# Optimization experiments

Hardware: AMD Instinct MI355X
Metric: run time of the kernel (lower is better)

Reference implementation:

```python
import jax, jax.numpy as jnp
import numpy as np

B, N, E, H = 1, 4096, 256, 4
D = E // H  # 64


def setup_inputs() -> dict:
    key = jax.random.key(0)
    ks = jax.random.split(key, 16)
    s = lambda fan_in: 1.0 / np.sqrt(fan_in)
    inp = {
        "x": jax.random.normal(ks[0], (B, N, E), dtype=jnp.float32),
        "encoding": jax.random.normal(ks[1], (2, 1, 1, N, D), dtype=jnp.float32),
        # Wqkv: Linear(E, 3E)
        "Wqkv_w": jax.random.uniform(ks[2], (3 * E, E), jnp.float32, -s(E), s(E)),
        "Wqkv_b": jax.random.uniform(ks[3], (3 * E,), jnp.float32, -s(E), s(E)),
        # out_proj: Linear(E, E)
        "out_w": jax.random.uniform(ks[4], (E, E), jnp.float32, -s(E), s(E)),
        "out_b": jax.random.uniform(ks[5], (E,), jnp.float32, -s(E), s(E)),
        # ffn[0]: Linear(2E, 2E)
        "ffn1_w": jax.random.uniform(ks[6], (2 * E, 2 * E), jnp.float32, -s(2 * E), s(2 * E)),
        "ffn1_b": jax.random.uniform(ks[7], (2 * E,), jnp.float32, -s(2 * E), s(2 * E)),
        # ffn[1]: LayerNorm(2E)
        "ln_g": jnp.ones((2 * E,), jnp.float32),
        "ln_b": jnp.zeros((2 * E,), jnp.float32),
        # ffn[3]: Linear(2E, E)
        "ffn2_w": jax.random.uniform(ks[8], (E, 2 * E), jnp.float32, -s(2 * E), s(2 * E)),
        "ffn2_b": jax.random.uniform(ks[9], (E,), jnp.float32, -s(2 * E), s(2 * E)),
    }
    return inp


def _rotate_half(t):
    # t: (B, H, N, D) -> pairwise rotate along last dim
    t2 = t.reshape(B, H, -1, D // 2, 2)
    t2 = jnp.stack((-t2[..., 1], t2[..., 0]), axis=-1)
    return t2.reshape(B, H, -1, D)


def _layernorm(x, g, b, eps=1e-5):
    mu = jnp.mean(x, axis=-1, keepdims=True)
    var = jnp.mean(jnp.square(x - mu), axis=-1, keepdims=True)
    return (x - mu) * jax.lax.rsqrt(var + eps) * g + b


def reference(x, encoding, Wqkv_w, Wqkv_b, out_w, out_b,
              ffn1_w, ffn1_b, ln_g, ln_b, ffn2_w, ffn2_b):
    # fused QKV projection; last dim layout is (H, D, 3)
    qkv = x @ Wqkv_w.T + Wqkv_b                       # (B, N, 3E)
    qkv = qkv.reshape(B, N, H, D, 3).transpose(0, 2, 1, 3, 4)  # (B, H, N, D, 3)
    q, k, v = qkv[..., 0], qkv[..., 1], qkv[..., 2]
    # cached rotary embedding: t*cos + rotate_half(t)*sin
    q = q * encoding[0] + _rotate_half(q) * encoding[1]
    k = k * encoding[0] + _rotate_half(k) * encoding[1]
    # scaled dot-product attention (no mask)
    scores = jnp.einsum("bhqd,bhkd->bhqk", q, k) / np.sqrt(D).astype(np.float32)
    probs = jax.nn.softmax(scores, axis=-1)
    ctx = jnp.einsum("bhqk,bhkd->bhqd", probs, v)     # (B, H, N, D)
    ctx = ctx.transpose(0, 2, 1, 3).reshape(B, N, E)
    message = ctx @ out_w.T + out_b
    # concat-FFN with residual
    h = jnp.concatenate((x, message), axis=-1)        # (B, N, 2E)
    h = h @ ffn1_w.T + ffn1_b
    h = _layernorm(h, ln_g, ln_b)
    h = jax.nn.gelu(h, approximate=False)
    h = h @ ffn2_w.T + ffn2_b
    return x + h
```

## Files before the change

### kernel.cpp

```cpp
#include <hip/hip_runtime.h>
#include <math.h>

#define NTOK 4096
#define EMB  256
#define NH   4
#define HD   64

typedef unsigned short u16;
typedef __attribute__((ext_vector_type(8))) __bf16 bf16x8;
typedef __attribute__((ext_vector_type(4))) float f32x4;

__device__ __forceinline__ u16 f2bf(float f) {
    union { float f; unsigned u; } v; v.f = f;
    unsigned b = v.u;
    b += 0x7FFFu + ((b >> 16) & 1u);
    return (u16)(b >> 16);
}
__device__ __forceinline__ float bf2f(u16 u) {
    union { unsigned u; float f; } v; v.u = ((unsigned)u) << 16;
    return v.f;
}

__global__ __launch_bounds__(256) void prep(
    const float4* __restrict__ w0, const float4* __restrict__ w1,
    const float4* __restrict__ w2, const float4* __restrict__ w3,
    u16* __restrict__ wb,
    const float4* __restrict__ x4, u16* __restrict__ xb, u16* __restrict__ catb)
{
    const int bid = blockIdx.x;
    if (bid < 640) {
        const int f = bid * 256 + threadIdx.x;
        float4 v;
        if      (f <  49152) v = w0[f];
        else if (f <  65536) v = w1[f - 49152];
        else if (f < 131072) v = w2[f - 65536];
        else                 v = w3[f - 131072];
        uint2 o;
        o.x = (unsigned)f2bf(v.x) | ((unsigned)f2bf(v.y) << 16);
        o.y = (unsigned)f2bf(v.z) | ((unsigned)f2bf(v.w) << 16);
        *(uint2*)(wb + (size_t)f * 4) = o;
    } else {
        const int f = (bid - 640) * 256 + threadIdx.x;
        float4 v = x4[f];
        uint2 o;
        o.x = (unsigned)f2bf(v.x) | ((unsigned)f2bf(v.y) << 16);
        o.y = (unsigned)f2bf(v.z) | ((unsigned)f2bf(v.w) << 16);
        *(uint2*)(xb + (size_t)f * 4) = o;
        const int row = f >> 6, c = (f & 63) * 4;
        *(uint2*)(catb + (size_t)row * 512 + c) = o;
    }
}

__global__ __launch_bounds__(256) void gemm_bf16_abt(
    const u16* __restrict__ A,
    const u16* __restrict__ B,
    const float* __restrict__ bias,
    const float* __restrict__ resid, int ldr,
    float* __restrict__ Cf, u16* __restrict__ Cb, int ldc, int K)
{
    const int t = threadIdx.x, w = t >> 6, l = t & 63;
    const int lg = l >> 4, li = l & 15;
    const int row0 = blockIdx.y * 64 + w * 16;
    const int col0 = blockIdx.x * 64;

    f32x4 acc[4];
    #pragma unroll
    for (int nb = 0; nb < 4; ++nb) acc[nb] = (f32x4){0.f, 0.f, 0.f, 0.f};

    const u16* Ap = A + (size_t)(row0 + li) * K + lg * 8;
    const u16* Bp = B + (size_t)(col0 + li) * K + lg * 8;

    #pragma unroll 2
    for (int k0 = 0; k0 < K; k0 += 32) {
        bf16x8 a = *(const bf16x8*)(Ap + k0);
        #pragma unroll
        for (int nb = 0; nb < 4; ++nb) {
            bf16x8 b = *(const bf16x8*)(Bp + (size_t)nb * 16 * K + k0);
            acc[nb] = __builtin_amdgcn_mfma_f32_16x16x32_bf16(a, b, acc[nb], 0, 0, 0);
        }
    }

    #pragma unroll
    for (int nb = 0; nb < 4; ++nb) {
        const int col = col0 + nb * 16 + li;
        const float bs = bias[col];
        #pragma unroll
        for (int p = 0; p < 4; ++p) {
            const int row = row0 + lg * 4 + p;
            float v = acc[nb][p] + bs;
            if (resid) v += resid[(size_t)row * ldr + col];
            if (Cf) Cf[(size_t)row * ldc + col] = v;
            else    Cb[(size_t)row * ldc + col] = f2bf(v);
        }
    }
}

__global__ __launch_bounds__(256) void qkv_post(
    const u16* __restrict__ qkvb, const float* __restrict__ enc,
    unsigned* __restrict__ Qb, unsigned* __restrict__ Kb, u16* __restrict__ Vt)
{
    __shared__ u16 lds[64 * 66];
    const int bid = blockIdx.x;
    if (bid < 2048) {
        const int gid = bid * 256 + threadIdx.x;
        const int h   = gid >> 17;
        const int rem = gid & (NTOK * 32 - 1);
        const int n   = rem >> 5;
        const int p   = rem & 31;
        const int d0  = p * 2;

        const u16* base = qkvb + (size_t)n * 768 + h * 192 + d0 * 3;
        const float q0v = bf2f(base[0]), k0 = bf2f(base[1]);
        const float q1  = bf2f(base[3]), k1 = bf2f(base[4]);

        float2 c01 = *(const float2*)(enc + (size_t)n * 64 + d0);
        float2 s01 = *(const float2*)(enc + (size_t)NTOK * 64 + (size_t)n * 64 + d0);

        const float qo0 = (q0v * c01.x - q1 * s01.x) * 0.125f;
        const float qo1 = (q1 * c01.y + q0v * s01.y) * 0.125f;
        const float ko0 = k0 * c01.x - k1 * s01.x;
        const float ko1 = k1 * c01.y + k0 * s01.y;

        const size_t oidx = ((size_t)(h * NTOK + n) << 5) + p;
        Qb[oidx] = (unsigned)f2bf(qo0) | ((unsigned)f2bf(qo1) << 16);
        Kb[oidx] = (unsigned)f2bf(ko0) | ((unsigned)f2bf(ko1) << 16);
    } else {
        const int vb = bid - 2048;
        const int h  = vb >> 6;
        const int nt = vb & 63;
        const int t  = threadIdx.x;

        {
            const int nl = t & 63, dg = t >> 6;
            const u16* src = qkvb + (size_t)(nt * 64 + nl) * 768 + h * 192 + dg * 48 + 2;
            #pragma unroll
            for (int i = 0; i < 16; ++i)
                lds[(dg * 16 + i) * 66 + nl] = src[3 * i];
        }
        __syncthreads();
        {
            const int d = t >> 2, nc = t & 3;
            __align__(16) u16 us[16];
            #pragma unroll
            for (int i = 0; i < 16; ++i) us[i] = lds[d * 66 + nc * 16 + i];
            u16* dst = Vt + ((size_t)(h * 64 + d) << 12) + nt * 64 + nc * 16;
            *(uint4*)(dst)     = *(uint4*)(us);
            *(uint4*)(dst + 8) = *(uint4*)(us + 8);
        }
    }
}

__global__ __launch_bounds__(256, 4) void flash_attn_v4(
    const u16* __restrict__ Qb, const u16* __restrict__ Kb,
    const u16* __restrict__ Vt, u16* __restrict__ ctxb)
{
    __shared__ char  Plds[4 * 2048];
    __shared__ float Obuf[16 * 64];
    __shared__ float Mbuf[16], Lbuf[16];

    const int t  = threadIdx.x;
    const int wk = t >> 6;
    const int l  = t & 63;
    const int lg = l >> 4, li = l & 15;
    const int h  = blockIdx.y;
    const int q0 = blockIdx.x * 16;

    char* Pw = Plds + wk * 2048;

    bf16x8 QA[2];
    #pragma unroll
    for (int kh = 0; kh < 2; ++kh)
        QA[kh] = *(const bf16x8*)(Qb +
            ((size_t)(h * NTOK + q0 + li) << 6) + kh * 32 + lg * 8);

    f32x4 OA[4];
    float mrun[4], lrun[4];
    #pragma unroll
    for (int p = 0; p < 4; ++p) { mrun[p] = -1e30f; lrun[p] = 0.f; }
    #pragma unroll
    for (int db = 0; db < 4; ++db) OA[db] = (f32x4){0.f, 0.f, 0.f, 0.f};

    for (int it = 0; it < 16; ++it) {
        const int kt = (wk << 10) + (it << 6);

        bf16x8 KB[4][2], VB[4][2];
        #pragma unroll
        for (int kb = 0; kb < 4; ++kb)
            #pragma unroll
            for (int kh = 0; kh < 2; ++kh)
                KB[kb][kh] = *(const bf16x8*)(Kb +
                    ((size_t)(h * NTOK + kt + kb * 16 + li) << 6) + kh * 32 + lg * 8);
        #pragma unroll
        for (int db = 0; db < 4; ++db)
            #pragma unroll
            for (int kh = 0; kh < 2; ++kh)
                VB[db][kh] = *(const bf16x8*)(Vt +
                    ((size_t)(h * 64 + db * 16 + li) << 12) + kt + kh * 32 + lg * 8);

        f32x4 SA[4];
        #pragma unroll
        for (int kb = 0; kb < 4; ++kb) {
            f32x4 z = (f32x4){0.f, 0.f, 0.f, 0.f};
            z = __builtin_amdgcn_mfma_f32_16x16x32_bf16(QA[0], KB[kb][0], z, 0, 0, 0);
            SA[kb] = __builtin_amdgcn_mfma_f32_16x16x32_bf16(QA[1], KB[kb][1], z, 0, 0, 0);
        }

        #pragma unroll
        for (int p = 0; p < 4; ++p) {
            float mx = fmaxf(fmaxf(SA[0][p], SA[1][p]), fmaxf(SA[2][p], SA[3][p]));
            #pragma unroll
            for (int sh = 1; sh < 16; sh <<= 1)
                mx = fmaxf(mx, __shfl_xor(mx, sh));
            const float mo = mrun[p];
            const float mn = fmaxf(mo, mx);
            const float corr = __expf(mo - mn);
            mrun[p] = mn;
            float pv[4], ps = 0.f;
            #pragma unroll
            for (int kb = 0; kb < 4; ++kb) {
                pv[kb] = __expf(SA[kb][p] - mn);
                ps += pv[kb];
            }
            lrun[p] = lrun[p] * corr + ps;
            #pragma unroll
            for (int db = 0; db < 4; ++db) OA[db][p] *= corr;

            const int ql = lg * 4 + p;
            #pragma unroll
            for (int kb = 0; kb < 4; ++kb) {
                const int kl = kb * 16 + li;
                *(u16*)(Pw + ql * 128 + ((kl * 2) ^ ((ql & 7) << 4))) = f2bf(pv[kb]);
            }
        }

        #pragma unroll
        for (int kh = 0; kh < 2; ++kh) {
            const int ql = li;
            bf16x8 PA = *(const bf16x8*)(Pw + ql * 128 +
                            ((kh * 64 + lg * 16) ^ ((ql & 7) << 4)));
            #pragma unroll
            for (int db = 0; db < 4; ++db)
                OA[db] = __builtin_amdgcn_mfma_f32_16x16x32_bf16(
                    PA, VB[db][kh], OA[db], 0, 0, 0);
        }
    }

    #pragma unroll
    for (int p = 0; p < 4; ++p) {
        float ps = lrun[p];
        #pragma unroll
        for (int sh = 1; sh < 16; sh <<= 1) ps += __shfl_xor(ps, sh);
        lrun[p] = ps;
    }

    if (wk == 0) {
        #pragma unroll
        for (int p = 0; p < 4; ++p) {
            const int q = lg * 4 + p;
            #pragma unroll
            for (int db = 0; db < 4; ++db)
                Obuf[q * 64 + db * 16 + li] = OA[db][p];
            if (li == 0) { Mbuf[q] = mrun[p]; Lbuf[q] = lrun[p]; }
        }
    }
    #pragma unroll
    for (int wv = 1; wv < 4; ++wv) {
        __syncthreads();
        if (wk == wv) {
            #pragma unroll
            for (int p = 0; p < 4; ++p) {
                const int q = lg * 4 + p;
                const float Mo = Mbuf[q], Lo = Lbuf[q];
                const float mn = fmaxf(Mo, mrun[p]);
                const float a  = __expf(Mo - mn);
                const float b  = __expf(mrun[p] - mn);
                #pragma unroll
                for (int db = 0; db < 4; ++db) {
                    const int idx = q * 64 + db * 16 + li;
                    Obuf[idx] = Obuf[idx] * a + OA[db][p] * b;
                }
                if (li == 0) { Mbuf[q] = mn; Lbuf[q] = Lo * a + lrun[p] * b; }
            }
        }
    }
    __syncthreads();

    {
        const int q = t >> 4, dc = (t & 15) * 4;
        const float rl = 1.f / Lbuf[q];
        uint2 ov;
        ov.x = (unsigned)f2bf(Obuf[q * 64 + dc + 0] * rl) |
               ((unsigned)f2bf(Obuf[q * 64 + dc + 1] * rl) << 16);
        ov.y = (unsigned)f2bf(Obuf[q * 64 + dc + 2] * rl) |
               ((unsigned)f2bf(Obuf[q * 64 + dc + 3] * rl) << 16);
        *(uint2*)(ctxb + (size_t)(q0 + q) * EMB + h * 64 + dc) = ov;
    }
}

__global__ __launch_bounds__(256) void ln_gelu_v2(
    const u16* __restrict__ h1b, const float* __restrict__ g,
    const float* __restrict__ b, u16* __restrict__ h2b)
{
    const int wid = threadIdx.x >> 6, l = threadIdx.x & 63;
    const int row = blockIdx.x * 4 + wid;

    uint4 hv = *(const uint4*)(h1b + (size_t)row * 512 + l * 8);
    const unsigned* hw = (const unsigned*)&hv;
    float v[8];
    #pragma unroll
    for (int j = 0; j < 4; ++j) {
        v[2 * j]     = bf2f((u16)(hw[j] & 0xffff));
        v[2 * j + 1] = bf2f((u16)(hw[j] >> 16));
    }

    float s = 0.f;
    #pragma unroll
    for (int i = 0; i < 8; ++i) s += v[i];
    #pragma unroll
    for (int sh = 1; sh < 64; sh <<= 1) s += __shfl_xor(s, sh);
    const float mu = s * (1.f / 512.f);

    float d[8], vs = 0.f;
    #pragma unroll
    for (int i = 0; i < 8; ++i) { d[i] = v[i] - mu; vs += d[i] * d[i]; }
    #pragma unroll
    for (int sh = 1; sh < 64; sh <<= 1) vs += __shfl_xor(vs, sh);
    const float rstd = rsqrtf(vs * (1.f / 512.f) + 1e-5f);

    float4 g0 = *(const float4*)(g + l * 8);
    float4 g1 = *(const float4*)(g + l * 8 + 4);
    float4 b0 = *(const float4*)(b + l * 8);
    float4 b1 = *(const float4*)(b + l * 8 + 4);
    float gg[8] = {g0.x, g0.y, g0.z, g0.w, g1.x, g1.y, g1.z, g1.w};
    float bb[8] = {b0.x, b0.y, b0.z, b0.w, b1.x, b1.y, b1.z, b1.w};

    uint4 ov;
    unsigned* op = (unsigned*)&ov;
    #pragma unroll
    for (int j = 0; j < 4; ++j) {
        float y0 = d[2 * j] * rstd * gg[2 * j] + bb[2 * j];
        float y1 = d[2 * j + 1] * rstd * gg[2 * j + 1] + bb[2 * j + 1];
        float o0 = 0.5f * y0 * (1.f + erff(y0 * 0.70710678118654752f));
        float o1 = 0.5f * y1 * (1.f + erff(y1 * 0.70710678118654752f));
        op[j] = (unsigned)f2bf(o0) | ((unsigned)f2bf(o1) << 16);
    }
    *(uint4*)(h2b + (size_t)row * 512 + l * 8) = ov;
}

extern "C" void kernel_launch(void* const* d_in, const int* in_sizes, int n_in,
                              void* d_out, int out_size, void* d_ws, size_t ws_size,
                              hipStream_t stream)
{
    const float* x      = (const float*)d_in[0];
    const float* enc    = (const float*)d_in[1];
    const float* Wqkv_w = (const float*)d_in[2];
    const float* Wqkv_b = (const float*)d_in[3];
    const float* out_w  = (const float*)d_in[4];
    const float* out_b  = (const float*)d_in[5];
    const float* ffn1_w = (const float*)d_in[6];
    const float* ffn1_b = (const float*)d_in[7];
    const float* ln_g   = (const float*)d_in[8];
    const float* ln_b   = (const float*)d_in[9];
    const float* ffn2_w = (const float*)d_in[10];
    const float* ffn2_b = (const float*)d_in[11];
    float* out = (float*)d_out;
    float* ws  = (float*)d_ws;

    u16*   catb = (u16*)(ws);
    u16*   wb   = (u16*)(ws + 1048576);
    u16*   Qb   = (u16*)(ws + 1376256);
    u16*   Kb   = (u16*)(ws + 1900544);
    u16*   Vt   = (u16*)(ws + 2424832);
    u16*   ctxb = (u16*)(ws + 2949120);
    u16*   qkvb = (u16*)(ws + 3473408);
    u16*   h1b  = (u16*)(ws + 3473408);
    u16*   xb   = (u16*)(ws + 5570560);
    u16*   h2b  = (u16*)(ws + 5570560);

    u16* Wqkvb = wb;
    u16* outwb = wb + 196608;
    u16* ffn1b = wb + 262144;
    u16* ffn2b = wb + 524288;

    prep<<<1664, 256, 0, stream>>>((const float4*)Wqkv_w, (const float4*)out_w,
                                   (const float4*)ffn1_w, (const float4*)ffn2_w, wb,
                                   (const float4*)x, xb, catb);
    gemm_bf16_abt<<<dim3(12, 64), 256, 0, stream>>>(xb, Wqkvb, Wqkv_b,
                                                    nullptr, 0, nullptr, qkvb, 768, 256);
    qkv_post<<<2304, 256, 0, stream>>>(qkvb, enc, (unsigned*)Qb, (unsigned*)Kb, Vt);
    flash_attn_v4<<<dim3(256, NH), 256, 0, stream>>>(Qb, Kb, Vt, ctxb);
    gemm_bf16_abt<<<dim3(4, 64), 256, 0, stream>>>(ctxb, outwb, out_b,
                                                   nullptr, 0, nullptr, catb + 256, 512, 256);
    gemm_bf16_abt<<<dim3(8, 64), 256, 0, stream>>>(catb, ffn1b, ffn1_b,
                                                   nullptr, 0, nullptr, h1b, 512, 512);
    ln_gelu_v2<<<1024, 256, 0, stream>>>(h1b, ln_g, ln_b, h2b);
    gemm_bf16_abt<<<dim3(4, 64), 256, 0, stream>>>(h2b, ffn2b, ffn2_b,
                                                   x, 256, out, nullptr, 256, 512);
}
```

Measured before the change: 280.8 us.

## Double query tile per wave in attention and GEMM, add register prefetching

Flash attention now handles 32 query rows per block (two 16-row MFMA tiles per wave), so each K/V fragment loaded is reused twice, and it double-buffers the next K/V tile in registers. The GEMM likewise computes 128 rows per block with two A fragments per wave and register-prefetches the next K-slice. The output write is widened to 16-byte stores. This cuts global load traffic per FLOP and hides load latency, at the cost of more registers, lower occupancy (launch bounds 2 for attention), and half as many blocks.

New measurement: 229.2 us. 1.22x faster.

```diff
diff --git a/kernel.cpp b/kernel.cpp
--- a/kernel.cpp
+++ b/kernel.cpp
@@ -51,7 +51,7 @@
     }
 }
 
-__global__ __launch_bounds__(256) void gemm_bf16_abt(
+__global__ __launch_bounds__(256, 4) void gemm_bf16_v2(
     const u16* __restrict__ A,
     const u16* __restrict__ B,
     const float* __restrict__ bias,
@@ -60,39 +60,66 @@
 {
     const int t = threadIdx.x, w = t >> 6, l = t & 63;
     const int lg = l >> 4, li = l & 15;
-    const int row0 = blockIdx.y * 64 + w * 16;
+    const int row0 = blockIdx.y * 128 + w * 32;
     const int col0 = blockIdx.x * 64;
 
-    f32x4 acc[4];
-    #pragma unroll
-    for (int nb = 0; nb < 4; ++nb) acc[nb] = (f32x4){0.f, 0.f, 0.f, 0.f};
-
-    const u16* Ap = A + (size_t)(row0 + li) * K + lg * 8;
-    const u16* Bp = B + (size_t)(col0 + li) * K + lg * 8;
-
-    #pragma unroll 2
-    for (int k0 = 0; k0 < K; k0 += 32) {
-        bf16x8 a = *(const bf16x8*)(Ap + k0);
+    f32x4 acc[2][4];
+    #pragma unroll
+    for (int m = 0; m < 2; ++m)
+        #pragma unroll
+        for (int nb = 0; nb < 4; ++nb) acc[m][nb] = (f32x4){0.f, 0.f, 0.f, 0.f};
+
+    const u16* Ap0 = A + (size_t)(row0 + li) * K + lg * 8;
+    const u16* Ap1 = Ap0 + (size_t)16 * K;
+    const u16* Bp  = B + (size_t)(col0 + li) * K + lg * 8;
+
+    bf16x8 a0c = *(const bf16x8*)(Ap0);
+    bf16x8 a1c = *(const bf16x8*)(Ap1);
+    bf16x8 b0c = *(const bf16x8*)(Bp);
+    bf16x8 b1c = *(const bf16x8*)(Bp + (size_t)16 * K);
+    bf16x8 b2c = *(const bf16x8*)(Bp + (size_t)32 * K);
+    bf16x8 b3c = *(const bf16x8*)(Bp + (size_t)48 * K);
+    bf16x8 a0n, a1n, b0n, b1n, b2n, b3n;
+
+#define GSTEP(a0x,a1x,b0x,b1x,b2x,b3x, a0y,a1y,b0y,b1y,b2y,b3y, KC) do { \
+    const int kn_ = ((KC) + 32 < K) ? (KC) + 32 : (KC); \
+    a0y = *(const bf16x8*)(Ap0 + kn_); \
+    a1y = *(const bf16x8*)(Ap1 + kn_); \
+    b0y = *(const bf16x8*)(Bp + kn_); \
+    b1y = *(const bf16x8*)(Bp + (size_t)16 * K + kn_); \
+    b2y = *(const bf16x8*)(Bp + (size_t)32 * K + kn_); \
+    b3y = *(const bf16x8*)(Bp + (size_t)48 * K + kn_); \
+    acc[0][0] = __builtin_amdgcn_mfma_f32_16x16x32_bf16(a0x, b0x, acc[0][0], 0, 0, 0); \
+    acc[0][1] = __builtin_amdgcn_mfma_f32_16x16x32_bf16(a0x, b1x, acc[0][1], 0, 0, 0); \
+    acc[0][2] = __builtin_amdgcn_mfma_f32_16x16x32_bf16(a0x, b2x, acc[0][2], 0, 0, 0); \
+    acc[0][3] = __builtin_amdgcn_mfma_f32_16x16x32_bf16(a0x, b3x, acc[0][3], 0, 0, 0); \
+    acc[1][0] = __builtin_amdgcn_mfma_f32_16x16x32_bf16(a1x, b0x, acc[1][0], 0, 0, 0); \
+    acc[1][1] = __builtin_amdgcn_mfma_f32_16x16x32_bf16(a1x, b1x, acc[1][1], 0, 0, 0); \
+    acc[1][2] = __builtin_amdgcn_mfma_f32_16x16x32_bf16(a1x, b2x, acc[1][2], 0, 0, 0); \
+    acc[1][3] = __builtin_amdgcn_mfma_f32_16x16x32_bf16(a1x, b3x, acc[1][3], 0, 0, 0); \
+} while (0)
+
+    for (int k0 = 0; k0 < K; k0 += 64) {
+        GSTEP(a0c,a1c,b0c,b1c,b2c,b3c, a0n,a1n,b0n,b1n,b2n,b3n, k0);
+        GSTEP(a0n,a1n,b0n,b1n,b2n,b3n, a0c,a1c,b0c,b1c,b2c,b3c, k0 + 32);
+    }
+#undef GSTEP
+
+    #pragma unroll
+    for (int m = 0; m < 2; ++m)
         #pragma unroll
         for (int nb = 0; nb < 4; ++nb) {
-            bf16x8 b = *(const bf16x8*)(Bp + (size_t)nb * 16 * K + k0);
-            acc[nb] = __builtin_amdgcn_mfma_f32_16x16x32_bf16(a, b, acc[nb], 0, 0, 0);
+            const int col = col0 + nb * 16 + li;
+            const float bs = bias[col];
+            #pragma unroll
+            for (int p = 0; p < 4; ++p) {
+                const int row = row0 + m * 16 + lg * 4 + p;
+                float v = acc[m][nb][p] + bs;
+                if (resid) v += resid[(size_t)row * ldr + col];
+                if (Cf) Cf[(size_t)row * ldc + col] = v;
+                else    Cb[(size_t)row * ldc + col] = f2bf(v);
+            }
         }
-    }
-
-    #pragma unroll
-    for (int nb = 0; nb < 4; ++nb) {
-        const int col = col0 + nb * 16 + li;
-        const float bs = bias[col];
-        #pragma unroll
-        for (int p = 0; p < 4; ++p) {
-            const int row = row0 + lg * 4 + p;
-            float v = acc[nb][p] + bs;
-            if (resid) v += resid[(size_t)row * ldr + col];
-            if (Cf) Cf[(size_t)row * ldc + col] = v;
-            else    Cb[(size_t)row * ldc + col] = f2bf(v);
-        }
-    }
 }
 
 __global__ __launch_bounds__(256) void qkv_post(
@@ -150,150 +177,182 @@
     }
 }
 
-__global__ __launch_bounds__(256, 4) void flash_attn_v4(
+__global__ __launch_bounds__(256, 2) void flash_attn_v5(
     const u16* __restrict__ Qb, const u16* __restrict__ Kb,
     const u16* __restrict__ Vt, u16* __restrict__ ctxb)
 {
-    __shared__ char  Plds[4 * 2048];
-    __shared__ float Obuf[16 * 64];
-    __shared__ float Mbuf[16], Lbuf[16];
+    __shared__ char  Plds[4 * 4096];
+    __shared__ float Obuf[32 * 64];
+    __shared__ float Mbuf[32], Lbuf[32];
 
     const int t  = threadIdx.x;
     const int wk = t >> 6;
     const int l  = t & 63;
     const int lg = l >> 4, li = l & 15;
     const int h  = blockIdx.y;
-    const int q0 = blockIdx.x * 16;
-
-    char* Pw = Plds + wk * 2048;
-
-    bf16x8 QA[2];
-    #pragma unroll
-    for (int kh = 0; kh < 2; ++kh)
-        QA[kh] = *(const bf16x8*)(Qb +
-            ((size_t)(h * NTOK + q0 + li) << 6) + kh * 32 + lg * 8);
-
-    f32x4 OA[4];
-    float mrun[4], lrun[4];
-    #pragma unroll
-    for (int p = 0; p < 4; ++p) { mrun[p] = -1e30f; lrun[p] = 0.f; }
-    #pragma unroll
-    for (int db = 0; db < 4; ++db) OA[db] = (f32x4){0.f, 0.f, 0.f, 0.f};
-
-    for (int it = 0; it < 16; ++it) {
-        const int kt = (wk << 10) + (it << 6);
-
-        bf16x8 KB[4][2], VB[4][2];
+    const int q0 = blockIdx.x * 32;
+
+    char* Pw = Plds + wk * 4096;
+
+    bf16x8 QA[2][2];
+    #pragma unroll
+    for (int Mb = 0; Mb < 2; ++Mb)
+        #pragma unroll
+        for (int kh = 0; kh < 2; ++kh)
+            QA[Mb][kh] = *(const bf16x8*)(Qb +
+                ((size_t)(h * NTOK + q0 + Mb * 16 + li) << 6) + kh * 32 + lg * 8);
+
+    f32x4 OA[2][4];
+    float mrun[2][4], lrun[2][4];
+    #pragma unroll
+    for (int Mb = 0; Mb < 2; ++Mb) {
+        #pragma unroll
+        for (int p = 0; p < 4; ++p) { mrun[Mb][p] = -1e30f; lrun[Mb][p] = 0.f; }
+        #pragma unroll
+        for (int db = 0; db < 4; ++db) OA[Mb][db] = (f32x4){0.f, 0.f, 0.f, 0.f};
+    }
+
+    bf16x8 K0f[4][2], V0f[4][2], K1f[4][2], V1f[4][2];
+
+    {
+        const int kt0 = wk << 10;
         #pragma unroll
         for (int kb = 0; kb < 4; ++kb)
             #pragma unroll
-            for (int kh = 0; kh < 2; ++kh)
-                KB[kb][kh] = *(const bf16x8*)(Kb +
-                    ((size_t)(h * NTOK + kt + kb * 16 + li) << 6) + kh * 32 + lg * 8);
-        #pragma unroll
-        for (int db = 0; db < 4; ++db)
-            #pragma unroll
-            for (int kh = 0; kh < 2; ++kh)
-                VB[db][kh] = *(const bf16x8*)(Vt +
-                    ((size_t)(h * 64 + db * 16 + li) << 12) + kt + kh * 32 + lg * 8);
-
-        f32x4 SA[4];
-        #pragma unroll
-        for (int kb = 0; kb < 4; ++kb) {
-            f32x4 z = (f32x4){0.f, 0.f, 0.f, 0.f};
-            z = __builtin_amdgcn_mfma_f32_16x16x32_bf16(QA[0], KB[kb][0], z, 0, 0, 0);
-            SA[kb] = __builtin_amdgcn_mfma_f32_16x16x32_bf16(QA[1], KB[kb][1], z, 0, 0, 0);
+            for (int kh = 0; kh < 2; ++kh) {
+                K0f[kb][kh] = *(const bf16x8*)(Kb +
+                    ((size_t)(h * NTOK + kt0 + kb * 16 + li) << 6) + kh * 32 + lg * 8);
+                V0f[kb][kh] = *(const bf16x8*)(Vt +
+                    ((size_t)(h * 64 + kb * 16 + li) << 12) + kt0 + kh * 32 + lg * 8);
+            }
+    }
+
+#define FITER(KC, VC, KN, VN, IT) do { \
+    const int itn_ = ((IT) < 15) ? (IT) + 1 : (IT); \
+    const int ktn_ = (wk << 10) + (itn_ << 6); \
+    _Pragma("unroll") \
+    for (int kb = 0; kb < 4; ++kb) { \
+        _Pragma("unroll") \
+        for (int kh = 0; kh < 2; ++kh) { \
+            KN[kb][kh] = *(const bf16x8*)(Kb + \
+                ((size_t)(h * NTOK + ktn_ + kb * 16 + li) << 6) + kh * 32 + lg * 8); \
+            VN[kb][kh] = *(const bf16x8*)(Vt + \
+                ((size_t)(h * 64 + kb * 16 + li) << 12) + ktn_ + kh * 32 + lg * 8); \
+        } \
+    } \
+    f32x4 SA_[2][4]; \
+    _Pragma("unroll") \
+    for (int Mb = 0; Mb < 2; ++Mb) { \
+        _Pragma("unroll") \
+        for (int kb = 0; kb < 4; ++kb) { \
+            f32x4 z_ = (f32x4){0.f, 0.f, 0.f, 0.f}; \
+            z_ = __builtin_amdgcn_mfma_f32_16x16x32_bf16(QA[Mb][0], KC[kb][0], z_, 0, 0, 0); \
+            SA_[Mb][kb] = __builtin_amdgcn_mfma_f32_16x16x32_bf16(QA[Mb][1], KC[kb][1], z_, 0, 0, 0); \
+        } \
+    } \
+    _Pragma("unroll") \
+    for (int Mb = 0; Mb < 2; ++Mb) { \
+        _Pragma("unroll") \
+        for (int p = 0; p < 4; ++p) { \
+            float mx_ = fmaxf(fmaxf(SA_[Mb][0][p], SA_[Mb][1][p]), \
+                              fmaxf(SA_[Mb][2][p], SA_[Mb][3][p])); \
+            _Pragma("unroll") \
+            for (int sh = 1; sh < 16; sh <<= 1) mx_ = fmaxf(mx_, __shfl_xor(mx_, sh)); \
+            const float mo_ = mrun[Mb][p]; \
+            const float mn_ = fmaxf(mo_, mx_); \
+            const float corr_ = __expf(mo_ - mn_); \
+            mrun[Mb][p] = mn_; \
+            float pe0_ = __expf(SA_[Mb][0][p] - mn_); \
+            float pe1_ = __expf(SA_[Mb][1][p] - mn_); \
+            float pe2_ = __expf(SA_[Mb][2][p] - mn_); \
+            float pe3_ = __expf(SA_[Mb][3][p] - mn_); \
+            lrun[Mb][p] = lrun[Mb][p] * corr_ + (pe0_ + pe1_ + pe2_ + pe3_); \
+            _Pragma("unroll") \
+            for (int db = 0; db < 4; ++db) OA[Mb][db][p] *= corr_; \
+            const int ql_ = Mb * 16 + lg * 4 + p; \
+            *(u16*)(Pw + ql_ * 128 + (((0 * 16 + li) * 2) ^ ((ql_ & 7) << 4))) = f2bf(pe0_); \
+            *(u16*)(Pw + ql_ * 128 + (((1 * 16 + li) * 2) ^ ((ql_ & 7) << 4))) = f2bf(pe1_); \
+            *(u16*)(Pw + ql_ * 128 + (((2 * 16 + li) * 2) ^ ((ql_ & 7) << 4))) = f2bf(pe2_); \
+            *(u16*)(Pw + ql_ * 128 + (((3 * 16 + li) * 2) ^ ((ql_ & 7) << 4))) = f2bf(pe3_); \
+        } \
+    } \
+    _Pragma("unroll") \
+    for (int Mb = 0; Mb < 2; ++Mb) { \
+        _Pragma("unroll") \
+        for (int kh = 0; kh < 2; ++kh) { \
+            const int ql_ = Mb * 16 + li; \
+            bf16x8 PA_ = *(const bf16x8*)(Pw + ql_ * 128 + \
+                            ((kh * 64 + lg * 16) ^ ((ql_ & 7) << 4))); \
+            _Pragma("unroll") \
+            for (int db = 0; db < 4; ++db) \
+                OA[Mb][db] = __builtin_amdgcn_mfma_f32_16x16x32_bf16( \
+                    PA_, VC[db][kh], OA[Mb][db], 0, 0, 0); \
+        } \
+    } \
+} while (0)
+
+    for (int it = 0; it < 16; it += 2) {
+        FITER(K0f, V0f, K1f, V1f, it);
+        FITER(K1f, V1f, K0f, V0f, it + 1);
+    }
+#undef FITER
+
+    #pragma unroll
+    for (int Mb = 0; Mb < 2; ++Mb)
+        #pragma unroll
+        for (int p = 0; p < 4; ++p) {
+            float ps = lrun[Mb][p];
+            #pragma unroll
+            for (int sh = 1; sh < 16; sh <<= 1) ps += __shfl_xor(ps, sh);
+            lrun[Mb][p] = ps;
         }
 
-        #pragma unroll
-        for (int p = 0; p < 4; ++p) {
-            float mx = fmaxf(fmaxf(SA[0][p], SA[1][p]), fmaxf(SA[2][p], SA[3][p]));
-            #pragma unroll
-            for (int sh = 1; sh < 16; sh <<= 1)
-                mx = fmaxf(mx, __shfl_xor(mx, sh));
-            const float mo = mrun[p];
-            const float mn = fmaxf(mo, mx);
-            const float corr = __expf(mo - mn);
-            mrun[p] = mn;
-            float pv[4], ps = 0.f;
-            #pragma unroll
-            for (int kb = 0; kb < 4; ++kb) {
-                pv[kb] = __expf(SA[kb][p] - mn);
-                ps += pv[kb];
+    if (wk == 0) {
+        #pragma unroll
+        for (int Mb = 0; Mb < 2; ++Mb)
+            #pragma unroll
+            for (int p = 0; p < 4; ++p) {
+                const int q = Mb * 16 + lg * 4 + p;
+                #pragma unroll
+                for (int db = 0; db < 4; ++db)
+                    Obuf[q * 64 + db * 16 + li] = OA[Mb][db][p];
+                if (li == 0) { Mbuf[q] = mrun[Mb][p]; Lbuf[q] = lrun[Mb][p]; }
             }
-            lrun[p] = lrun[p] * corr + ps;
-            #pragma unroll
-            for (int db = 0; db < 4; ++db) OA[db][p] *= corr;
-
-            const int ql = lg * 4 + p;
-            #pragma unroll
-            for (int kb = 0; kb < 4; ++kb) {
-                const int kl = kb * 16 + li;
-                *(u16*)(Pw + ql * 128 + ((kl * 2) ^ ((ql & 7) << 4))) = f2bf(pv[kb]);
-            }
-        }
-
-        #pragma unroll
-        for (int kh = 0; kh < 2; ++kh) {
-            const int ql = li;
-            bf16x8 PA = *(const bf16x8*)(Pw + ql * 128 +
-                            ((kh * 64 + lg * 16) ^ ((ql & 7) << 4)));
-            #pragma unroll
-            for (int db = 0; db < 4; ++db)
-                OA[db] = __builtin_amdgcn_mfma_f32_16x16x32_bf16(
-                    PA, VB[db][kh], OA[db], 0, 0, 0);
-        }
-    }
-
-    #pragma unroll
-    for (int p = 0; p < 4; ++p) {
-        float ps = lrun[p];
-        #pragma unroll
-        for (int sh = 1; sh < 16; sh <<= 1) ps += __shfl_xor(ps, sh);
-        lrun[p] = ps;
-    }
-
-    if (wk == 0) {
-        #pragma unroll
-        for (int p = 0; p < 4; ++p) {
-            const int q = lg * 4 + p;
-            #pragma unroll
-            for (int db = 0; db < 4; ++db)
-                Obuf[q * 64 + db * 16 + li] = OA[db][p];
-            if (li == 0) { Mbuf[q] = mrun[p]; Lbuf[q] = lrun[p]; }
-        }
     }
     #pragma unroll
     for (int wv = 1; wv < 4; ++wv) {
         __syncthreads();
         if (wk == wv) {
             #pragma unroll
-            for (int p = 0; p < 4; ++p) {
-                const int q = lg * 4 + p;
-                const float Mo = Mbuf[q], Lo = Lbuf[q];
-                const float mn = fmaxf(Mo, mrun[p]);
-                const float a  = __expf(Mo - mn);
-                const float b  = __expf(mrun[p] - mn);
+            for (int Mb = 0; Mb < 2; ++Mb)
                 #pragma unroll
-                for (int db = 0; db < 4; ++db) {
-                    const int idx = q * 64 + db * 16 + li;
-                    Obuf[idx] = Obuf[idx] * a + OA[db][p] * b;
+                for (int p = 0; p < 4; ++p) {
+                    const int q = Mb * 16 + lg * 4 + p;
+                    const float Mo = Mbuf[q], Lo = Lbuf[q];
+                    const float mn = fmaxf(Mo, mrun[Mb][p]);
+                    const float a  = __expf(Mo - mn);
+                    const float b  = __expf(mrun[Mb][p] - mn);
+                    #pragma unroll
+                    for (int db = 0; db < 4; ++db) {
+                        const int idx = q * 64 + db * 16 + li;
+                        Obuf[idx] = Obuf[idx] * a + OA[Mb][db][p] * b;
+                    }
+                    if (li == 0) { Mbuf[q] = mn; Lbuf[q] = Lo * a + lrun[Mb][p] * b; }
                 }
-                if (li == 0) { Mbuf[q] = mn; Lbuf[q] = Lo * a + lrun[p] * b; }
-            }
         }
     }
     __syncthreads();
 
     {
-        const int q = t >> 4, dc = (t & 15) * 4;
+        const int q = t >> 3, dc = (t & 7) * 8;
         const float rl = 1.f / Lbuf[q];
-        uint2 ov;
-        ov.x = (unsigned)f2bf(Obuf[q * 64 + dc + 0] * rl) |
-               ((unsigned)f2bf(Obuf[q * 64 + dc + 1] * rl) << 16);
-        ov.y = (unsigned)f2bf(Obuf[q * 64 + dc + 2] * rl) |
-               ((unsigned)f2bf(Obuf[q * 64 + dc + 3] * rl) << 16);
-        *(uint2*)(ctxb + (size_t)(q0 + q) * EMB + h * 64 + dc) = ov;
+        uint4 ov;
+        unsigned* op = (unsigned*)&ov;
+        #pragma unroll
+        for (int i = 0; i < 8; i += 2)
+            op[i >> 1] = (unsigned)f2bf(Obuf[q * 64 + dc + i] * rl) |
+                         ((unsigned)f2bf(Obuf[q * 64 + dc + i + 1] * rl) << 16);
+        *(uint4*)(ctxb + (size_t)(q0 + q) * EMB + h * 64 + dc) = ov;
     }
 }
 
@@ -385,15 +444,15 @@
     prep<<<1664, 256, 0, stream>>>((const float4*)Wqkv_w, (const float4*)out_w,
                                    (const float4*)ffn1_w, (const float4*)ffn2_w, wb,
                                    (const float4*)x, xb, catb);
-    gemm_bf16_abt<<<dim3(12, 64), 256, 0, stream>>>(xb, Wqkvb, Wqkv_b,
-                                                    nullptr, 0, nullptr, qkvb, 768, 256);
+    gemm_bf16_v2<<<dim3(12, 32), 256, 0, stream>>>(xb, Wqkvb, Wqkv_b,
+                                                   nullptr, 0, nullptr, qkvb, 768, 256);
     qkv_post<<<2304, 256, 0, stream>>>(qkvb, enc, (unsigned*)Qb, (unsigned*)Kb, Vt);
-    flash_attn_v4<<<dim3(256, NH), 256, 0, stream>>>(Qb, Kb, Vt, ctxb);
-    gemm_bf16_abt<<<dim3(4, 64), 256, 0, stream>>>(ctxb, outwb, out_b,
-                                                   nullptr, 0, nullptr, catb + 256, 512, 256);
-    gemm_bf16_abt<<<dim3(8, 64), 256, 0, stream>>>(catb, ffn1b, ffn1_b,
-                                                   nullptr, 0, nullptr, h1b, 512, 512);
+    flash_attn_v5<<<dim3(128, NH), 256, 0, stream>>>(Qb, Kb, Vt, ctxb);
+    gemm_bf16_v2<<<dim3(4, 32), 256, 0, stream>>>(ctxb, outwb, out_b,
+                                                  nullptr, 0, nullptr, catb + 256, 512, 256);
+    gemm_bf16_v2<<<dim3(8, 32), 256, 0, stream>>>(catb, ffn1b, ffn1_b,
+                                                  nullptr, 0, nullptr, h1b, 512, 512);
     ln_gelu_v2<<<1024, 256, 0, stream>>>(h1b, ln_g, ln_b, h2b);
-    gemm_bf16_abt<<<dim3(4, 64), 256, 0, stream>>>(h2b, ffn2b, ffn2_b,
-                                                   x, 256, out, nullptr, 256, 512);
-}
+    gemm_bf16_v2<<<dim3(4, 32), 256, 0, stream>>>(h2b, ffn2b, ffn2_b,
+                                                  x, 256, out, nullptr, 256, 512);
+}
```

## Double-buffer GEMM operand loads and widen flash attention to 32 queries per block

Applied to the files above, without the earlier changes.

The GEMM loop now software-pipelines its global loads, fetching the next K-slice's A and B fragments into a second register set while MFMAs run on the current one. It also adds an occupancy hint to the launch bounds. The attention kernel goes to 512 threads covering 32 queries with 8 waves, so each K/V tile loaded by a key-split wave position serves two query groups across the block. V loads are moved after the QK^T MFMAs to shorten register live ranges. The costs are more registers for double buffering and twice the LDS per attention block, which may reduce occupancy.

Result: faster. 272.3 us (-3.0%).

```diff
diff --git a/kernel.cpp b/kernel.cpp
--- a/kernel.cpp
+++ b/kernel.cpp
@@ -51,7 +51,7 @@
     }
 }
 
-__global__ __launch_bounds__(256) void gemm_bf16_abt(
+__global__ __launch_bounds__(256, 4) void gemm_bf16_v3(
     const u16* __restrict__ A,
     const u16* __restrict__ B,
     const float* __restrict__ bias,
@@ -70,15 +70,31 @@
     const u16* Ap = A + (size_t)(row0 + li) * K + lg * 8;
     const u16* Bp = B + (size_t)(col0 + li) * K + lg * 8;
 
-    #pragma unroll 2
-    for (int k0 = 0; k0 < K; k0 += 32) {
-        bf16x8 a = *(const bf16x8*)(Ap + k0);
-        #pragma unroll
-        for (int nb = 0; nb < 4; ++nb) {
-            bf16x8 b = *(const bf16x8*)(Bp + (size_t)nb * 16 * K + k0);
-            acc[nb] = __builtin_amdgcn_mfma_f32_16x16x32_bf16(a, b, acc[nb], 0, 0, 0);
-        }
-    }
+    bf16x8 ac  = *(const bf16x8*)(Ap);
+    bf16x8 b0c = *(const bf16x8*)(Bp);
+    bf16x8 b1c = *(const bf16x8*)(Bp + (size_t)16 * K);
+    bf16x8 b2c = *(const bf16x8*)(Bp + (size_t)32 * K);
+    bf16x8 b3c = *(const bf16x8*)(Bp + (size_t)48 * K);
+    bf16x8 an, b0n, b1n, b2n, b3n;
+
+#define GSTEP(ax,b0x,b1x,b2x,b3x, ay,b0y,b1y,b2y,b3y, KC) do { \
+    const int kn_ = ((KC) + 32 < K) ? (KC) + 32 : (KC); \
+    ay  = *(const bf16x8*)(Ap + kn_); \
+    b0y = *(const bf16x8*)(Bp + kn_); \
+    b1y = *(const bf16x8*)(Bp + (size_t)16 * K + kn_); \
+    b2y = *(const bf16x8*)(Bp + (size_t)32 * K + kn_); \
+    b3y = *(const bf16x8*)(Bp + (size_t)48 * K + kn_); \
+    acc[0] = __builtin_amdgcn_mfma_f32_16x16x32_bf16(ax, b0x, acc[0], 0, 0, 0); \
+    acc[1] = __builtin_amdgcn_mfma_f32_16x16x32_bf16(ax, b1x, acc[1], 0, 0, 0); \
+    acc[2] = __builtin_amdgcn_mfma_f32_16x16x32_bf16(ax, b2x, acc[2], 0, 0, 0); \
+    acc[3] = __builtin_amdgcn_mfma_f32_16x16x32_bf16(ax, b3x, acc[3], 0, 0, 0); \
+} while (0)
+
+    for (int k0 = 0; k0 < K; k0 += 64) {
+        GSTEP(ac,b0c,b1c,b2c,b3c, an,b0n,b1n,b2n,b3n, k0);
+        GSTEP(an,b0n,b1n,b2n,b3n, ac,b0c,b1c,b2c,b3c, k0 + 32);
+    }
+#undef GSTEP
 
     #pragma unroll
     for (int nb = 0; nb < 4; ++nb) {
@@ -150,28 +166,29 @@
     }
 }
 
-__global__ __launch_bounds__(256, 4) void flash_attn_v4(
+__global__ __launch_bounds__(512, 4) void flash_attn_v6(
     const u16* __restrict__ Qb, const u16* __restrict__ Kb,
     const u16* __restrict__ Vt, u16* __restrict__ ctxb)
 {
-    __shared__ char  Plds[4 * 2048];
-    __shared__ float Obuf[16 * 64];
-    __shared__ float Mbuf[16], Lbuf[16];
+    __shared__ char  Plds[8 * 2048];
+    __shared__ float Obuf[32 * 64];
+    __shared__ float Mbuf[32], Lbuf[32];
 
     const int t  = threadIdx.x;
-    const int wk = t >> 6;
+    const int w  = t >> 6;
+    const int wq = w >> 2, wk = w & 3;
     const int l  = t & 63;
     const int lg = l >> 4, li = l & 15;
     const int h  = blockIdx.y;
-    const int q0 = blockIdx.x * 16;
-
-    char* Pw = Plds + wk * 2048;
+    const int q0 = blockIdx.x * 32;
+
+    char* Pw = Plds + w * 2048;
 
     bf16x8 QA[2];
     #pragma unroll
     for (int kh = 0; kh < 2; ++kh)
         QA[kh] = *(const bf16x8*)(Qb +
-            ((size_t)(h * NTOK + q0 + li) << 6) + kh * 32 + lg * 8);
+            ((size_t)(h * NTOK + q0 + wq * 16 + li) << 6) + kh * 32 + lg * 8);
 
     f32x4 OA[4];
     float mrun[4], lrun[4];
@@ -183,19 +200,13 @@
     for (int it = 0; it < 16; ++it) {
         const int kt = (wk << 10) + (it << 6);
 
-        bf16x8 KB[4][2], VB[4][2];
+        bf16x8 KB[4][2];
         #pragma unroll
         for (int kb = 0; kb < 4; ++kb)
             #pragma unroll
             for (int kh = 0; kh < 2; ++kh)
                 KB[kb][kh] = *(const bf16x8*)(Kb +
                     ((size_t)(h * NTOK + kt + kb * 16 + li) << 6) + kh * 32 + lg * 8);
-        #pragma unroll
-        for (int db = 0; db < 4; ++db)
-            #pragma unroll
-            for (int kh = 0; kh < 2; ++kh)
-                VB[db][kh] = *(const bf16x8*)(Vt +
-                    ((size_t)(h * 64 + db * 16 + li) << 12) + kt + kh * 32 + lg * 8);
 
         f32x4 SA[4];
         #pragma unroll
@@ -204,6 +215,14 @@
             z = __builtin_amdgcn_mfma_f32_16x16x32_bf16(QA[0], KB[kb][0], z, 0, 0, 0);
             SA[kb] = __builtin_amdgcn_mfma_f32_16x16x32_bf16(QA[1], KB[kb][1], z, 0, 0, 0);
         }
+
+        bf16x8 VB[4][2];
+        #pragma unroll
+        for (int db = 0; db < 4; ++db)
+            #pragma unroll
+            for (int kh = 0; kh < 2; ++kh)
+                VB[db][kh] = *(const bf16x8*)(Vt +
+                    ((size_t)(h * 64 + db * 16 + li) << 12) + kt + kh * 32 + lg * 8);
 
         #pragma unroll
         for (int p = 0; p < 4; ++p) {
@@ -256,7 +275,7 @@
     if (wk == 0) {
         #pragma unroll
         for (int p = 0; p < 4; ++p) {
-            const int q = lg * 4 + p;
+            const int q = wq * 16 + lg * 4 + p;
             #pragma unroll
             for (int db = 0; db < 4; ++db)
                 Obuf[q * 64 + db * 16 + li] = OA[db][p];
@@ -269,7 +288,7 @@
         if (wk == wv) {
             #pragma unroll
             for (int p = 0; p < 4; ++p) {
-                const int q = lg * 4 + p;
+                const int q = wq * 16 + lg * 4 + p;
                 const float Mo = Mbuf[q], Lo = Lbuf[q];
                 const float mn = fmaxf(Mo, mrun[p]);
                 const float a  = __expf(Mo - mn);
@@ -385,15 +404,15 @@
     prep<<<1664, 256, 0, stream>>>((const float4*)Wqkv_w, (const float4*)out_w,
                                    (const float4*)ffn1_w, (const float4*)ffn2_w, wb,
                                    (const float4*)x, xb, catb);
-    gemm_bf16_abt<<<dim3(12, 64), 256, 0, stream>>>(xb, Wqkvb, Wqkv_b,
-                                                    nullptr, 0, nullptr, qkvb, 768, 256);
+    gemm_bf16_v3<<<dim3(12, 64), 256, 0, stream>>>(xb, Wqkvb, Wqkv_b,
+                                                   nullptr, 0, nullptr, qkvb, 768, 256);
     qkv_post<<<2304, 256, 0, stream>>>(qkvb, enc, (unsigned*)Qb, (unsigned*)Kb, Vt);
-    flash_attn_v4<<<dim3(256, NH), 256, 0, stream>>>(Qb, Kb, Vt, ctxb);
-    gemm_bf16_abt<<<dim3(4, 64), 256, 0, stream>>>(ctxb, outwb, out_b,
-                                                   nullptr, 0, nullptr, catb + 256, 512, 256);
-    gemm_bf16_abt<<<dim3(8, 64), 256, 0, stream>>>(catb, ffn1b, ffn1_b,
-                                                   nullptr, 0, nullptr, h1b, 512, 512);
+    flash_attn_v6<<<dim3(128, NH), 512, 0, stream>>>(Qb, Kb, Vt, ctxb);
+    gemm_bf16_v3<<<dim3(4, 64), 256, 0, stream>>>(ctxb, outwb, out_b,
+                                                  nullptr, 0, nullptr, catb + 256, 512, 256);
+    gemm_bf16_v3<<<dim3(8, 64), 256, 0, stream>>>(catb, ffn1b, ffn1_b,
+                                                  nullptr, 0, nullptr, h1b, 512, 512);
     ln_gelu_v2<<<1024, 256, 0, stream>>>(h1b, ln_g, ln_b, h2b);
-    gemm_bf16_abt<<<dim3(4, 64), 256, 0, stream>>>(h2b, ffn2b, ffn2_b,
-                                                   x, 256, out, nullptr, 256, 512);
-}
+    gemm_bf16_v3<<<dim3(4, 64), 256, 0, stream>>>(h2b, ffn2b, ffn2_b,
+                                                  x, 256, out, nullptr, 256, 512);
+}
```
